# Kernel tuning notes

Measured on AMD Instinct MI355X. Metric: run time of the kernel, lower is better.

Reference implementation:

```python
import jax, jax.numpy as jnp
import numpy as np

N, E, D = 50000, 400000, 64
L, NA, NS = 5, 4, 3            # layers, num aggregators, num scalers
ATOM_C, ATOM_V = 9, 64         # OGB-style atom feature columns / vocab
BOND_C, BOND_V = 3, 8
EPS = 1e-5
AVG_LOG = float(np.log(9.0))   # avg_d['log'] = ln(avg_degree + 1), avg_degree = 8


def setup_inputs() -> dict:
    key = jax.random.key(0)
    ks = jax.random.split(key, 8)
    x = jax.random.randint(ks[0], (N, ATOM_C), 0, ATOM_V)
    edge_index = jax.random.randint(ks[1], (2, E), 0, N)
    edge_attr = jax.random.randint(ks[2], (E, BOND_C), 0, BOND_V)
    init = lambda k, shape, fan: (jax.random.normal(k, shape, jnp.float32) / np.sqrt(fan))
    atom_emb = init(ks[3], (ATOM_C, ATOM_V, D), D)
    bond_emb = init(ks[4], (BOND_C, BOND_V, D), D)
    pre_W = init(ks[5], (L, 3 * D, D), 3 * D)                 # pretrans: Linear(3D -> D)
    pre_b = jnp.zeros((L, D), jnp.float32)
    post_W = init(ks[6], (L, (NA * NS + 1) * D, D), (NA * NS + 1) * D)  # posttrans: Linear(13D -> D)
    post_b = jnp.zeros((L, D), jnp.float32)
    return dict(x=x, edge_index=edge_index, edge_attr=edge_attr,
                atom_emb=atom_emb, bond_emb=bond_emb,
                pre_W=pre_W, pre_b=pre_b, post_W=post_W, post_b=post_b)


def reference(x, edge_index, edge_attr, atom_emb, bond_emb, pre_W, pre_b, post_W, post_b):
    src, dst = edge_index[0], edge_index[1]  # PyG: x_j = x[edge_index[0]], x_i = x[edge_index[1]]
    # Encoders: sum of per-column categorical embeddings (OGB Atom/BondEncoder)
    h0 = atom_emb[jnp.arange(ATOM_C)[None, :], x].sum(axis=1)        # [N, D]
    e = bond_emb[jnp.arange(BOND_C)[None, :], edge_attr].sum(axis=1)  # [E, D]
    # message input cat([x_i, x_j, edge_attr]) -- identical for every layer since
    # PNAGNN.forward never feeds layer output back in as x (faithful to source)
    z2 = jnp.concatenate([h0[dst], h0[src], e], axis=-1)              # [E, 3D]
    deg = jax.ops.segment_sum(jnp.ones((E,), jnp.float32), dst, num_segments=N)
    degc = jnp.maximum(deg, 1.0)[:, None]
    log_deg = jnp.log(jnp.maximum(deg, 1.0) + 1.0)[:, None]           # guard deg=0 for attenuation
    amp = log_deg / AVG_LOG
    att = AVG_LOG / log_deg
    has = (deg > 0)[:, None]
    h_in = h0
    for l in range(L):
        m = z2 @ pre_W[l] + pre_b[l]                                  # pretrans (1 layer, no act)
        s_sum = jax.ops.segment_sum(m, dst, num_segments=N)
        mean = s_sum / degc
        mx = jnp.where(has, jax.ops.segment_max(m, dst, num_segments=N), 0.0)
        mn = jnp.where(has, jax.ops.segment_min(m, dst, num_segments=N), 0.0)
        mean_sq = jax.ops.segment_sum(m * m, dst, num_segments=N) / degc
        var = jax.nn.relu(mean_sq - mean * mean)
        std = jnp.sqrt(var + EPS)
        agg = jnp.concatenate([mean, mx, mn, std], axis=-1)           # [N, 4D]
        scaled = jnp.concatenate([agg, agg * amp, agg * att], axis=-1)  # [N, 12D]
        hcat = jnp.concatenate([scaled, h0], axis=-1)                 # [N, 13D]
        out = hcat @ post_W[l] + post_b[l]                            # posttrans (1 layer, no act)
        h = out + h_in                                                # PNAGNN residual
        h_in = h
    return h
```

## Files before the change

### kernel.cpp

```cpp
#include <hip/hip_runtime.h>
#include <hip/hip_bf16.h>

#define NN 50000
#define NE 400000
#define AVG_LOG_F 2.1972245773362196f
#define EPSV 1e-5f

typedef __hip_bfloat16 bf16;
typedef __attribute__((ext_vector_type(8))) short short8v;
typedef __attribute__((ext_vector_type(4))) float f32x4;
typedef __attribute__((ext_vector_type(2))) _Float16 h2v;

__device__ __forceinline__ float b2f(bf16 v){ return __bfloat162float(v); }
__device__ __forceinline__ bf16  f2b(float v){ return __float2bfloat16(v); }
__device__ __forceinline__ short f2s(float v){
  bf16 b = __float2bfloat16(v);
  short s; __builtin_memcpy(&s, &b, 2); return s;
}
__device__ __forceinline__ short f2h(float v){
  _Float16 h = (_Float16)v;
  short s; __builtin_memcpy(&s, &h, 2); return s;
}

__global__ void k_h0(const int* __restrict__ x, const float* __restrict__ aemb,
                     bf16* __restrict__ h0b){
  int idx = blockIdx.x * 256 + threadIdx.x;
  if (idx >= NN * 64) return;
  int n = idx >> 6, d = idx & 63;
  float acc = 0.f;
  #pragma unroll
  for (int c = 0; c < 9; ++c){
    int a = x[n * 9 + c];
    acc += aemb[(c * 64 + a) * 64 + d];
  }
  h0b[idx] = f2b(acc);
}

__global__ void k_deg_code(const int* __restrict__ ei, const int* __restrict__ ea,
                           int* __restrict__ deg, int* __restrict__ code){
  int e = blockIdx.x * 256 + threadIdx.x;
  if (e >= NE) return;
  int dst = ei[NE + e];
  atomicAdd(&deg[dst], 1);
  code[e] = ea[e * 3] + 8 * ea[e * 3 + 1] + 64 * ea[e * 3 + 2];
}

__global__ void k_scan1(const int* __restrict__ deg, int* __restrict__ rowptr,
                        int* __restrict__ part){
  __shared__ int s[256];
  int t = threadIdx.x, i = blockIdx.x * 256 + t;
  int v = (i < NN) ? deg[i] : 0;
  s[t] = v; __syncthreads();
  for (int off = 1; off < 256; off <<= 1){
    int xv = (t >= off) ? s[t - off] : 0;
    __syncthreads();
    s[t] += xv;
    __syncthreads();
  }
  if (i < NN) rowptr[i] = s[t] - v;
  if (t == 255) part[blockIdx.x] = s[255];
}

__global__ void k_scan2(int* __restrict__ part, int nblk){
  __shared__ int s[256];
  int t = threadIdx.x;
  int v = (t < nblk) ? part[t] : 0;
  s[t] = v; __syncthreads();
  for (int off = 1; off < 256; off <<= 1){
    int xv = (t >= off) ? s[t - off] : 0;
    __syncthreads();
    s[t] += xv;
    __syncthreads();
  }
  if (t < nblk) part[t] = s[t] - v;
}

__global__ void k_scan3(int* __restrict__ rowptr, const int* __restrict__ part,
                        const int* __restrict__ deg, float* __restrict__ amp,
                        float* __restrict__ att){
  int i = blockIdx.x * 256 + threadIdx.x;
  if (i < NN){
    rowptr[i] += part[blockIdx.x];
    int d = deg[i];
    float ld = logf((float)max(d, 1) + 1.0f);
    amp[i] = ld / AVG_LOG_F;
    att[i] = AVG_LOG_F / ld;
  }
  if (i == 0) rowptr[NN] = NE;
}

__global__ void k_scatter(const int* __restrict__ ei, const int* __restrict__ code,
                          const int* __restrict__ rowptr, int* __restrict__ cursor,
                          int2* __restrict__ sedge){
  int e = blockIdx.x * 256 + threadIdx.x;
  if (e >= NE) return;
  int dst = ei[NE + e];
  int pos = rowptr[dst] + atomicAdd(&cursor[dst], 1);
  int2 v; v.x = ei[e] * 1280; v.y = code[e] * 640;
  sedge[pos] = v;
}

__global__ void k_ctab(const float* __restrict__ bemb, const float* __restrict__ preW,
                       _Float16* __restrict__ CTp){
  __shared__ float et[64];
  int cb = blockIdx.x, l = blockIdx.y, t = threadIdx.x;
  int a0 = cb & 7, a1 = (cb >> 3) & 7, a2 = (cb >> 6) & 7;
  et[t] = bemb[(0 * 8 + a0) * 64 + t] + bemb[(1 * 8 + a1) * 64 + t] + bemb[(2 * 8 + a2) * 64 + t];
  __syncthreads();
  float acc = 0.f;
  const float* W = preW + (l * 192 + 128) * 64;
  for (int k = 0; k < 64; ++k) acc += et[k] * W[k * 64 + t];
  char* base = (char*)CTp + (size_t)cb * 640;
  if (l < 4) *(short*)(base + t * 8 + l * 2) = f2h(acc);
  else       *(short*)(base + 512 + t * 2)   = f2h(acc);
}

__global__ void k_wtk(const float* __restrict__ postW, bf16* __restrict__ WtKf){
  int idx = blockIdx.x * 256 + threadIdx.x;
  if (idx >= 40 * 12 * 64 * 8) return;
  int s   = idx / 6144;
  int rem = idx % 6144;
  int gw  = rem / 512;
  int lane = (rem % 512) / 8;
  int j   = idx & 7;
  int g = gw >> 2, w4 = gw & 3;
  int kp = s * 32 + (lane >> 4) * 8 + j;
  int l = kp >> 8, kl = kp & 255;
  int c = w4 * 16 + (lane & 15);
  WtKf[idx] = f2b(postW[((size_t)l * 832 + g * 256 + kl) * 64 + c]);
}

__global__ void k_wtpre896(const float* __restrict__ preW, const float* __restrict__ preb,
                           const float* __restrict__ postW, const float* __restrict__ postb,
                           bf16* __restrict__ Wtp, float* __restrict__ bias896){
  int idx = blockIdx.x * 256 + threadIdx.x;
  if (idx < 896 * 64){
    int gc = idx >> 6, k = idx & 63;
    float v;
    if (gc < 320){
      int l = gc >> 6, c = gc & 63;
      v = preW[(size_t)(l * 192 + k) * 64 + c];
    } else if (gc < 832){
      int q = gc - 320, d = q >> 3, l = q & 7;
      v = (l < 5) ? preW[(size_t)(l * 192 + 64 + k) * 64 + d] : 0.f;
    } else {
      int c = gc - 832;
      float a = 0.f;
      #pragma unroll
      for (int l = 0; l < 5; ++l) a += postW[(size_t)(l * 832 + 768 + k) * 64 + c];
      v = a + ((k == c) ? 1.f : 0.f);
    }
    Wtp[idx] = f2b(v);
  }
  if (idx < 896){
    float b;
    if (idx < 320)      b = preb[(idx >> 6) * 64 + (idx & 63)];
    else if (idx < 832) b = 0.f;
    else {
      float a = 0.f;
      #pragma unroll
      for (int l = 0; l < 5; ++l) a += postb[l * 64 + (idx - 832)];
      b = a;
    }
    bias896[idx] = b;
  }
}

__global__ __launch_bounds__(256) void k_ab_mfma(const bf16* __restrict__ h0b,
                                                 const bf16* __restrict__ Wtp,
                                                 const float* __restrict__ bias896,
                                                 char* __restrict__ ABU,
                                                 float* __restrict__ out){
  __shared__ bf16 As[128][72];
  __shared__ bf16 Bs[128][72];
  const int t = threadIdx.x;
  const int n0 = blockIdx.x * 128;
  const int gc0 = blockIdx.y * 128;
  const int lane = t & 63, wid = t >> 6;
  const int rw = wid * 32;
  const short* H  = (const short*)h0b;
  const short* Wp = (const short*)Wtp;

  #pragma unroll
  for (int i = 0; i < 4; ++i){
    int idx = t + i * 256;
    int r = idx >> 3, ko = (idx & 7) * 8;
    int n = n0 + r;
    short8v v = short8v{0,0,0,0,0,0,0,0};
    if (n < NN) v = *(const short8v*)(H + (size_t)n * 64 + ko);
    *(short8v*)&As[r][ko] = v;
  }
  #pragma unroll
  for (int i = 0; i < 4; ++i){
    int idx = t + i * 256;
    int cc = idx >> 3, ko = (idx & 7) * 8;
    *(short8v*)&Bs[cc][ko] = *(const short8v*)(Wp + (size_t)(gc0 + cc) * 64 + ko);
  }
  __syncthreads();

  f32x4 acc[2][8] = {};
  #pragma unroll
  for (int kk = 0; kk < 2; ++kk){
    short8v af0 = *(const short8v*)&As[rw + (lane & 15)][kk * 32 + (lane >> 4) * 8];
    short8v af1 = *(const short8v*)&As[rw + 16 + (lane & 15)][kk * 32 + (lane >> 4) * 8];
    #pragma unroll
    for (int j = 0; j < 8; ++j){
      short8v bfj = *(const short8v*)&Bs[j * 16 + (lane & 15)][kk * 32 + (lane >> 4) * 8];
      acc[0][j] = __builtin_amdgcn_mfma_f32_16x16x32_bf16(af0, bfj, acc[0][j], 0, 0, 0);
      acc[1][j] = __builtin_amdgcn_mfma_f32_16x16x32_bf16(af1, bfj, acc[1][j], 0, 0, 0);
    }
  }

  #pragma unroll
  for (int i = 0; i < 2; ++i){
    #pragma unroll
    for (int r = 0; r < 4; ++r){
      int n = n0 + rw + i * 16 + (lane >> 4) * 4 + r;
      if (n >= NN) continue;
      char* nb = ABU + (size_t)n * 1280;
      #pragma unroll
      for (int j = 0; j < 8; ++j){
        int gc = gc0 + j * 16 + (lane & 15);
        float v = acc[i][j][r] + bias896[gc];
        if (gc < 320){
          *(short*)(nb + gc * 2) = f2h(v);
        } else if (gc < 832){
          int q = gc - 320, dd = q >> 3, l = q & 7;
          if (l < 4)       *(short*)(nb + 640 + dd * 8 + l * 2) = f2h(v);
          else if (l == 4) *(short*)(nb + 1152 + dd * 2)        = f2h(v);
        } else {
          out[(size_t)n * 64 + (gc - 832)] = v;
        }
      }
    }
  }
}

__global__ __launch_bounds__(1024, 2) void k_gather(const char* __restrict__ ABU,
                                                    const char* __restrict__ CTp,
                                                    const int* __restrict__ rowptr,
                                                    const int2* __restrict__ sedge,
                                                    const bf16* __restrict__ WtKf,
                                                    const float* __restrict__ amp,
                                                    const float* __restrict__ att,
                                                    float* __restrict__ out){
  __shared__ __align__(16) short ag[16][1288];
  const int t = threadIdx.x, lane = t & 63, wid = t >> 6;
  const int n = blockIdx.x * 16 + wid;
  const char* AB8 = ABU + 640;
  const char* AB2 = ABU + 1152;
  const char* CT8 = CTp;
  const char* CT2 = CTp + 512;

  int r0 = rowptr[n], r1 = rowptr[n + 1];
  float s[5]  = {0.f, 0.f, 0.f, 0.f, 0.f};
  float sq[5] = {0.f, 0.f, 0.f, 0.f, 0.f};
  const _Float16 FLO = (_Float16)(-65504.f);
  const _Float16 FHI = (_Float16)( 65504.f);
  h2v mx01 = h2v{FLO, FLO}, mx23 = h2v{FLO, FLO};
  h2v mn01 = h2v{FHI, FHI}, mn23 = h2v{FHI, FHI};
  float mx4 = -65504.f, mn4 = 65504.f;

  union U8 { uint2 u; h2v h[2]; };
  const int l8 = lane * 8, l2 = lane * 2;

  for (int j = r0; j < r1; j += 4){
    int rem = r1 - j;
    int2 e0 = sedge[j];
    int2 e1 = (rem > 1) ? sedge[j + 1] : e0;
    int2 e2 = (rem > 2) ? sedge[j + 2] : e0;
    int2 e3 = (rem > 3) ? sedge[j + 3] : e0;
    U8 a0, a1, a2, a3, c0, c1, c2, c3;
    unsigned short b0, b1, b2, b3, d0, d1, d2, d3;
    a0.u = *(const uint2*)(AB8 + e0.x + l8);  b0 = *(const unsigned short*)(AB2 + e0.x + l2);
    c0.u = *(const uint2*)(CT8 + e0.y + l8);  d0 = *(const unsigned short*)(CT2 + e0.y + l2);
    a1.u = *(const uint2*)(AB8 + e1.x + l8);  b1 = *(const unsigned short*)(AB2 + e1.x + l2);
    c1.u = *(const uint2*)(CT8 + e1.y + l8);  d1 = *(const unsigned short*)(CT2 + e1.y + l2);
    a2.u = *(const uint2*)(AB8 + e2.x + l8);  b2 = *(const unsigned short*)(AB2 + e2.x + l2);
    c2.u = *(const uint2*)(CT8 + e2.y + l8);  d2 = *(const unsigned short*)(CT2 + e2.y + l2);
    a3.u = *(const uint2*)(AB8 + e3.x + l8);  b3 = *(const unsigned short*)(AB2 + e3.x + l2);
    c3.u = *(const uint2*)(CT8 + e3.y + l8);  d3 = *(const unsigned short*)(CT2 + e3.y + l2);

    #define EDGE_ACC(A, C, BL, DL) {                                \
      h2v t01 = A.h[0] + C.h[0];                                    \
      h2v t23 = A.h[1] + C.h[1];                                    \
      _Float16 hb, hd;                                              \
      __builtin_memcpy(&hb, &BL, 2);                                \
      __builtin_memcpy(&hd, &DL, 2);                                \
      float f4 = (float)(hb + hd);                                  \
      mx01 = __builtin_elementwise_max(mx01, t01);                  \
      mx23 = __builtin_elementwise_max(mx23, t23);                  \
      mn01 = __builtin_elementwise_min(mn01, t01);                  \
      mn23 = __builtin_elementwise_min(mn23, t23);                  \
      mx4 = fmaxf(mx4, f4); mn4 = fminf(mn4, f4);                   \
      float f0 = (float)t01[0], f1 = (float)t01[1];                 \
      float f2 = (float)t23[0], f3 = (float)t23[1];                 \
      s[0] += f0; sq[0] = fmaf(f0, f0, sq[0]);                      \
      s[1] += f1; sq[1] = fmaf(f1, f1, sq[1]);                      \
      s[2] += f2; sq[2] = fmaf(f2, f2, sq[2]);                      \
      s[3] += f3; sq[3] = fmaf(f3, f3, sq[3]);                      \
      s[4] += f4; sq[4] = fmaf(f4, f4, sq[4]);                      \
    }
    EDGE_ACC(a0, c0, b0, d0);
    if (rem > 1) EDGE_ACC(a1, c1, b1, d1);
    if (rem > 2) EDGE_ACC(a2, c2, b2, d2);
    if (rem > 3) EDGE_ACC(a3, c3, b3, d3);
    #undef EDGE_ACC
  }

  float mx[5] = {(float)mx01[0], (float)mx01[1], (float)mx23[0], (float)mx23[1], mx4};
  float mn[5] = {(float)mn01[0], (float)mn01[1], (float)mn23[0], (float)mn23[1], mn4};

  int d = r1 - r0;
  float degc = (float)((d > 0) ? d : 1);
  const char* nb = ABU + (size_t)n * 1280;
  #pragma unroll
  for (int l = 0; l < 5; ++l){
    _Float16 Kh; __builtin_memcpy(&Kh, nb + l * 128 + lane * 2, 2);
    float K = (float)Kh;
    float mean = ((float)d * K + s[l]) / degc;
    float MX = (d > 0) ? (K + mx[l]) : 0.f;
    float MN = (d > 0) ? (K + mn[l]) : 0.f;
    float mu = s[l] / degc;
    float var = fmaxf(sq[l] / degc - mu * mu, 0.f);
    float sd = sqrtf(var + EPSV);
    ag[wid][l * 256 + lane]       = f2s(mean);
    ag[wid][l * 256 + 64 + lane]  = f2s(MX);
    ag[wid][l * 256 + 128 + lane] = f2s(MN);
    ag[wid][l * 256 + 192 + lane] = f2s(sd);
  }
  __syncthreads();

  if (wid >= 4) return;

  const char* pb = (const char*)WtKf + wid * 1024 + lane * 16;
  const short* agrow = &ag[lane & 15][(lane >> 4) * 8];
  f32x4 acc[3] = {};
  short8v Bx[3], By[3];

  #define LOADB(dst, sidx) { \
    _Pragma("unroll") for (int g = 0; g < 3; ++g) \
      dst[g] = *(const short8v*)(pb + (size_t)(sidx) * 12288 + g * 4096); }
  #define MFMA3(af, B) { \
    _Pragma("unroll") for (int g = 0; g < 3; ++g) \
      acc[g] = __builtin_amdgcn_mfma_f32_16x16x32_bf16(af, B[g], acc[g], 0, 0, 0); }

  LOADB(Bx, 0);
  for (int k = 0; k < 19; ++k){
    LOADB(By, 2 * k + 1);
    short8v af0 = *(const short8v*)(agrow + (2 * k) * 32);
    MFMA3(af0, Bx);
    LOADB(Bx, 2 * k + 2);
    short8v af1 = *(const short8v*)(agrow + (2 * k + 1) * 32);
    MFMA3(af1, By);
  }
  LOADB(By, 39);
  {
    short8v af0 = *(const short8v*)(agrow + 38 * 32);
    MFMA3(af0, Bx);
    short8v af1 = *(const short8v*)(agrow + 39 * 32);
    MFMA3(af1, By);
  }
  #undef LOADB
  #undef MFMA3

  #pragma unroll
  for (int r = 0; r < 4; ++r){
    int row = (lane >> 4) * 4 + r;
    int nn = blockIdx.x * 16 + row;
    float am = amp[nn], at = att[nn];
    int c = wid * 16 + (lane & 15);
    out[(size_t)nn * 64 + c] += acc[0][r] + am * acc[1][r] + at * acc[2][r];
  }
}

extern "C" void kernel_launch(void* const* d_in, const int* in_sizes, int n_in,
                              void* d_out, int out_size, void* d_ws, size_t ws_size,
                              hipStream_t stream){
  const int*   x     = (const int*)d_in[0];
  const int*   ei    = (const int*)d_in[1];
  const int*   ea    = (const int*)d_in[2];
  const float* aemb  = (const float*)d_in[3];
  const float* bemb  = (const float*)d_in[4];
  const float* preW  = (const float*)d_in[5];
  const float* preb  = (const float*)d_in[6];
  const float* postW = (const float*)d_in[7];
  const float* postb = (const float*)d_in[8];
  float* out = (float*)d_out;

  char* p = (char*)d_ws;
  auto alloc = [&](size_t bytes) -> char* {
    char* r = p;
    p += (bytes + 255) & ~(size_t)255;
    return r;
  };
  bf16*      h0b     = (bf16*)     alloc((size_t)NN * 64 * 2);
  char*      ABU     = (char*)     alloc((size_t)NN * 1280);
  int*       deg     = (int*)      alloc((size_t)NN * 4);
  int*       rowptr  = (int*)      alloc((size_t)(NN + 1) * 4);
  int*       cursor  = (int*)      alloc((size_t)NN * 4);
  float*     amp     = (float*)    alloc((size_t)NN * 4);
  float*     att     = (float*)    alloc((size_t)NN * 4);
  int*       code    = (int*)      alloc((size_t)NE * 4);
  int2*      sedge   = (int2*)     alloc((size_t)NE * 8);
  _Float16*  CTp     = (_Float16*) alloc((size_t)512 * 640);
  int*       part    = (int*)      alloc((size_t)256 * 4);
  bf16*      WtKf    = (bf16*)     alloc((size_t)40 * 12 * 64 * 8 * 2);
  bf16*      Wtp     = (bf16*)     alloc((size_t)896 * 64 * 2);
  float*     bias896 = (float*)    alloc((size_t)896 * 4);
  if ((size_t)(p - (char*)d_ws) > ws_size) return;

  hipMemsetAsync(deg, 0, (size_t)NN * 4, stream);
  hipMemsetAsync(cursor, 0, (size_t)NN * 4, stream);

  k_h0<<<dim3((NN * 64 + 255) / 256), 256, 0, stream>>>(x, aemb, h0b);
  k_deg_code<<<dim3((NE + 255) / 256), 256, 0, stream>>>(ei, ea, deg, code);
  int nblk = (NN + 255) / 256;
  k_scan1<<<dim3(nblk), 256, 0, stream>>>(deg, rowptr, part);
  k_scan2<<<dim3(1), 256, 0, stream>>>(part, nblk);
  k_scan3<<<dim3(nblk), 256, 0, stream>>>(rowptr, part, deg, amp, att);
  k_scatter<<<dim3((NE + 255) / 256), 256, 0, stream>>>(ei, code, rowptr, cursor, sedge);
  k_ctab<<<dim3(512, 5), 64, 0, stream>>>(bemb, preW, CTp);
  k_wtk<<<dim3((40 * 12 * 64 * 8 + 255) / 256), 256, 0, stream>>>(postW, WtKf);
  k_wtpre896<<<dim3((896 * 64 + 255) / 256), 256, 0, stream>>>(preW, preb, postW, postb,
                                                               Wtp, bias896);
  k_ab_mfma<<<dim3((NN + 127) / 128, 7), 256, 0, stream>>>(h0b, Wtp, bias896, ABU, out);
  k_gather<<<dim3(NN / 16), 1024, 0, stream>>>(ABU, (const char*)CTp, rowptr, sedge,
                                               WtKf, amp, att, out);
}
```

Baseline: 267.6 us.

## Split posttrans K-loop across all waves with LDS reduction

New measurement: 270.3 us. No clear change (+1.0%).

```diff
diff --git a/kernel.cpp b/kernel.cpp
--- a/kernel.cpp
+++ b/kernel.cpp
@@ -331,10 +331,9 @@
   }
   __syncthreads();
 
-  if (wid >= 4) return;
-
-  const char* pb = (const char*)WtKf + wid * 1024 + lane * 16;
-  const short* agrow = &ag[lane & 15][(lane >> 4) * 8];
+  const int cs = wid & 3, kq = wid >> 2;
+  const char* pb = (const char*)WtKf + cs * 1024 + (size_t)kq * 10 * 12288 + lane * 16;
+  const short* agq = &ag[lane & 15][(lane >> 4) * 8] + kq * 10 * 32;
   f32x4 acc[3] = {};
   short8v Bx[3], By[3];
 
@@ -346,23 +345,36 @@
       acc[g] = __builtin_amdgcn_mfma_f32_16x16x32_bf16(af, B[g], acc[g], 0, 0, 0); }
 
   LOADB(Bx, 0);
-  for (int k = 0; k < 19; ++k){
+  #pragma unroll
+  for (int k = 0; k < 5; ++k){
     LOADB(By, 2 * k + 1);
-    short8v af0 = *(const short8v*)(agrow + (2 * k) * 32);
+    short8v af0 = *(const short8v*)(agq + (2 * k) * 32);
     MFMA3(af0, Bx);
-    LOADB(Bx, 2 * k + 2);
-    short8v af1 = *(const short8v*)(agrow + (2 * k + 1) * 32);
-    MFMA3(af1, By);
-  }
-  LOADB(By, 39);
-  {
-    short8v af0 = *(const short8v*)(agrow + 38 * 32);
-    MFMA3(af0, Bx);
-    short8v af1 = *(const short8v*)(agrow + 39 * 32);
+    if (k < 4) LOADB(Bx, 2 * k + 2);
+    short8v af1 = *(const short8v*)(agq + (2 * k + 1) * 32);
     MFMA3(af1, By);
   }
   #undef LOADB
   #undef MFMA3
+
+  __syncthreads();
+  f32x4* red = (f32x4*)&ag[0][0];
+  if (wid >= 4){
+    #pragma unroll
+    for (int g = 0; g < 3; ++g)
+      red[((wid - 4) * 3 + g) * 64 + lane] = acc[g];
+    __syncthreads();
+    return;
+  }
+  __syncthreads();
+  #pragma unroll
+  for (int q = 0; q < 3; ++q){
+    #pragma unroll
+    for (int g = 0; g < 3; ++g){
+      f32x4 o = red[((q * 4 + wid) * 3 + g) * 64 + lane];
+      acc[g][0] += o[0]; acc[g][1] += o[1]; acc[g][2] += o[2]; acc[g][3] += o[3];
+    }
+  }
 
   #pragma unroll
   for (int r = 0; r < 4; ++r){
```

## Merge setup kernels and interleave five per-layer gather values into 12-byte records

Applied to the files above, without the earlier changes.

New measurement: 285.7 us. 6.8% more time.

```diff
diff --git a/kernel.cpp b/kernel.cpp
--- a/kernel.cpp
+++ b/kernel.cpp
@@ -11,7 +11,9 @@
 typedef __attribute__((ext_vector_type(4))) float f32x4;
 typedef __attribute__((ext_vector_type(2))) _Float16 h2v;
 
-__device__ __forceinline__ float b2f(bf16 v){ return __bfloat162float(v); }
+struct __attribute__((aligned(4))) u12 { unsigned x, y, z; };
+union P12 { u12 u; h2v h[3]; };
+
 __device__ __forceinline__ bf16  f2b(float v){ return __float2bfloat16(v); }
 __device__ __forceinline__ short f2s(float v){
   bf16 b = __float2bfloat16(v);
@@ -22,18 +24,102 @@
   short s; __builtin_memcpy(&s, &h, 2); return s;
 }
 
-__global__ void k_h0(const int* __restrict__ x, const float* __restrict__ aemb,
-                     bf16* __restrict__ h0b){
-  int idx = blockIdx.x * 256 + threadIdx.x;
-  if (idx >= NN * 64) return;
-  int n = idx >> 6, d = idx & 63;
-  float acc = 0.f;
-  #pragma unroll
-  for (int c = 0; c < 9; ++c){
-    int a = x[n * 9 + c];
-    acc += aemb[(c * 64 + a) * 64 + d];
-  }
-  h0b[idx] = f2b(acc);
+#define PB_H0  12500
+#define PB_Z   12891
+#define PB_CT  13403
+#define PB_WK  14363
+#define PB_END 14587
+
+__global__ __launch_bounds__(256) void k_pre(const int* __restrict__ x,
+                                             const float* __restrict__ aemb,
+                                             const float* __restrict__ bemb,
+                                             const float* __restrict__ preW,
+                                             const float* __restrict__ preb,
+                                             const float* __restrict__ postW,
+                                             const float* __restrict__ postb,
+                                             bf16* __restrict__ h0b,
+                                             int* __restrict__ deg, int* __restrict__ cursor,
+                                             char* __restrict__ CTp,
+                                             bf16* __restrict__ WtKf,
+                                             bf16* __restrict__ Wtp,
+                                             float* __restrict__ bias896){
+  __shared__ float et[64];
+  const int b = blockIdx.x, t = threadIdx.x;
+  if (b < PB_H0){
+    int idx = b * 256 + t;
+    int n = idx >> 6, d = idx & 63;
+    float acc = 0.f;
+    #pragma unroll
+    for (int c = 0; c < 9; ++c){
+      int a = x[n * 9 + c];
+      acc += aemb[(c * 64 + a) * 64 + d];
+    }
+    h0b[idx] = f2b(acc);
+  } else if (b < PB_Z){
+    int idx = (b - PB_H0) * 256 + t;
+    if (idx < NN) deg[idx] = 0;
+    else if (idx < 2 * NN) cursor[idx - NN] = 0;
+  } else if (b < PB_CT){
+    int cb = b - PB_Z;
+    if (t < 64){
+      int a0 = cb & 7, a1 = (cb >> 3) & 7, a2 = (cb >> 6) & 7;
+      et[t] = bemb[a0 * 64 + t] + bemb[(8 + a1) * 64 + t] + bemb[(16 + a2) * 64 + t];
+    }
+    __syncthreads();
+    char* base = CTp + (size_t)cb * 1024;
+    for (int w = t; w < 320; w += 256){
+      int l = w >> 6, dd = w & 63;
+      float acc = 0.f;
+      const float* W = preW + (l * 192 + 128) * 64;
+      for (int k = 0; k < 64; ++k) acc += et[k] * W[k * 64 + dd];
+      *(short*)(base + dd * 12 + l * 2) = f2h(acc);
+    }
+    if (t < 64) *(short*)(base + t * 12 + 10) = 0;
+  } else if (b < PB_WK){
+    int idx = (b - PB_CT) * 256 + t;
+    int s   = idx / 6144;
+    int rem = idx % 6144;
+    int gw  = rem / 512;
+    int lane = (rem % 512) / 8;
+    int j   = idx & 7;
+    int g = gw >> 2, w4 = gw & 3;
+    int kp = s * 32 + (lane >> 4) * 8 + j;
+    int l = kp >> 8, kl = kp & 255;
+    int c = w4 * 16 + (lane & 15);
+    WtKf[idx] = f2b(postW[((size_t)l * 832 + g * 256 + kl) * 64 + c]);
+  } else {
+    int idx = (b - PB_WK) * 256 + t;
+    {
+      int gc = idx >> 6, k = idx & 63;
+      float v;
+      if (gc < 320){
+        int l = gc >> 6, c = gc & 63;
+        v = preW[(size_t)(l * 192 + k) * 64 + c];
+      } else if (gc < 832){
+        int q = gc - 320, d = q >> 3, l = q & 7;
+        v = (l < 5) ? preW[(size_t)(l * 192 + 64 + k) * 64 + d] : 0.f;
+      } else {
+        int c = gc - 832;
+        float a = 0.f;
+        #pragma unroll
+        for (int l = 0; l < 5; ++l) a += postW[(size_t)(l * 832 + 768 + k) * 64 + c];
+        v = a + ((k == c) ? 1.f : 0.f);
+      }
+      Wtp[idx] = f2b(v);
+    }
+    if (idx < 896){
+      float bb;
+      if (idx < 320)      bb = preb[(idx >> 6) * 64 + (idx & 63)];
+      else if (idx < 832) bb = 0.f;
+      else {
+        float a = 0.f;
+        #pragma unroll
+        for (int l = 0; l < 5; ++l) a += postb[l * 64 + (idx - 832)];
+        bb = a;
+      }
+      bias896[idx] = bb;
+    }
+  }
 }
 
 __global__ void k_deg_code(const int* __restrict__ ei, const int* __restrict__ ea,
@@ -96,74 +182,8 @@
   if (e >= NE) return;
   int dst = ei[NE + e];
   int pos = rowptr[dst] + atomicAdd(&cursor[dst], 1);
-  int2 v; v.x = ei[e] * 1280; v.y = code[e] * 640;
+  int2 v; v.x = ei[e] * 2048 + 1024; v.y = code[e] * 1024;
   sedge[pos] = v;
-}
-
-__global__ void k_ctab(const float* __restrict__ bemb, const float* __restrict__ preW,
-                       _Float16* __restrict__ CTp){
-  __shared__ float et[64];
-  int cb = blockIdx.x, l = blockIdx.y, t = threadIdx.x;
-  int a0 = cb & 7, a1 = (cb >> 3) & 7, a2 = (cb >> 6) & 7;
-  et[t] = bemb[(0 * 8 + a0) * 64 + t] + bemb[(1 * 8 + a1) * 64 + t] + bemb[(2 * 8 + a2) * 64 + t];
-  __syncthreads();
-  float acc = 0.f;
-  const float* W = preW + (l * 192 + 128) * 64;
-  for (int k = 0; k < 64; ++k) acc += et[k] * W[k * 64 + t];
-  char* base = (char*)CTp + (size_t)cb * 640;
-  if (l < 4) *(short*)(base + t * 8 + l * 2) = f2h(acc);
-  else       *(short*)(base + 512 + t * 2)   = f2h(acc);
-}
-
-__global__ void k_wtk(const float* __restrict__ postW, bf16* __restrict__ WtKf){
-  int idx = blockIdx.x * 256 + threadIdx.x;
-  if (idx >= 40 * 12 * 64 * 8) return;
-  int s   = idx / 6144;
-  int rem = idx % 6144;
-  int gw  = rem / 512;
-  int lane = (rem % 512) / 8;
-  int j   = idx & 7;
-  int g = gw >> 2, w4 = gw & 3;
-  int kp = s * 32 + (lane >> 4) * 8 + j;
-  int l = kp >> 8, kl = kp & 255;
-  int c = w4 * 16 + (lane & 15);
-  WtKf[idx] = f2b(postW[((size_t)l * 832 + g * 256 + kl) * 64 + c]);
-}
-
-__global__ void k_wtpre896(const float* __restrict__ preW, const float* __restrict__ preb,
-                           const float* __restrict__ postW, const float* __restrict__ postb,
-                           bf16* __restrict__ Wtp, float* __restrict__ bias896){
-  int idx = blockIdx.x * 256 + threadIdx.x;
-  if (idx < 896 * 64){
-    int gc = idx >> 6, k = idx & 63;
-    float v;
-    if (gc < 320){
-      int l = gc >> 6, c = gc & 63;
-      v = preW[(size_t)(l * 192 + k) * 64 + c];
-    } else if (gc < 832){
-      int q = gc - 320, d = q >> 3, l = q & 7;
-      v = (l < 5) ? preW[(size_t)(l * 192 + 64 + k) * 64 + d] : 0.f;
-    } else {
-      int c = gc - 832;
-      float a = 0.f;
-      #pragma unroll
-      for (int l = 0; l < 5; ++l) a += postW[(size_t)(l * 832 + 768 + k) * 64 + c];
-      v = a + ((k == c) ? 1.f : 0.f);
-    }
-    Wtp[idx] = f2b(v);
-  }
-  if (idx < 896){
-    float b;
-    if (idx < 320)      b = preb[(idx >> 6) * 64 + (idx & 63)];
-    else if (idx < 832) b = 0.f;
-    else {
-      float a = 0.f;
-      #pragma unroll
-      for (int l = 0; l < 5; ++l) a += postb[l * 64 + (idx - 832)];
-      b = a;
-    }
-    bias896[idx] = b;
-  }
 }
 
 __global__ __launch_bounds__(256) void k_ab_mfma(const bf16* __restrict__ h0b,
@@ -217,7 +237,7 @@
     for (int r = 0; r < 4; ++r){
       int n = n0 + rw + i * 16 + (lane >> 4) * 4 + r;
       if (n >= NN) continue;
-      char* nb = ABU + (size_t)n * 1280;
+      char* nb = ABU + (size_t)n * 2048;
       #pragma unroll
       for (int j = 0; j < 8; ++j){
         int gc = gc0 + j * 16 + (lane & 15);
@@ -226,8 +246,7 @@
           *(short*)(nb + gc * 2) = f2h(v);
         } else if (gc < 832){
           int q = gc - 320, dd = q >> 3, l = q & 7;
-          if (l < 4)       *(short*)(nb + 640 + dd * 8 + l * 2) = f2h(v);
-          else if (l == 4) *(short*)(nb + 1152 + dd * 2)        = f2h(v);
+          if (l < 6) *(short*)(nb + 1024 + dd * 12 + l * 2) = f2h(v);
         } else {
           out[(size_t)n * 64 + (gc - 832)] = v;
         }
@@ -247,22 +266,16 @@
   __shared__ __align__(16) short ag[16][1288];
   const int t = threadIdx.x, lane = t & 63, wid = t >> 6;
   const int n = blockIdx.x * 16 + wid;
-  const char* AB8 = ABU + 640;
-  const char* AB2 = ABU + 1152;
-  const char* CT8 = CTp;
-  const char* CT2 = CTp + 512;
 
   int r0 = rowptr[n], r1 = rowptr[n + 1];
   float s[5]  = {0.f, 0.f, 0.f, 0.f, 0.f};
   float sq[5] = {0.f, 0.f, 0.f, 0.f, 0.f};
   const _Float16 FLO = (_Float16)(-65504.f);
   const _Float16 FHI = (_Float16)( 65504.f);
-  h2v mx01 = h2v{FLO, FLO}, mx23 = h2v{FLO, FLO};
-  h2v mn01 = h2v{FHI, FHI}, mn23 = h2v{FHI, FHI};
-  float mx4 = -65504.f, mn4 = 65504.f;
-
-  union U8 { uint2 u; h2v h[2]; };
-  const int l8 = lane * 8, l2 = lane * 2;
+  h2v mx01 = h2v{FLO, FLO}, mx23 = h2v{FLO, FLO}, mx45 = h2v{FLO, FLO};
+  h2v mn01 = h2v{FHI, FHI}, mn23 = h2v{FHI, FHI}, mn45 = h2v{FHI, FHI};
+
+  const int l12 = lane * 12;
 
   for (int j = r0; j < r1; j += 4){
     int rem = r1 - j;
@@ -270,50 +283,48 @@
     int2 e1 = (rem > 1) ? sedge[j + 1] : e0;
     int2 e2 = (rem > 2) ? sedge[j + 2] : e0;
     int2 e3 = (rem > 3) ? sedge[j + 3] : e0;
-    U8 a0, a1, a2, a3, c0, c1, c2, c3;
-    unsigned short b0, b1, b2, b3, d0, d1, d2, d3;
-    a0.u = *(const uint2*)(AB8 + e0.x + l8);  b0 = *(const unsigned short*)(AB2 + e0.x + l2);
-    c0.u = *(const uint2*)(CT8 + e0.y + l8);  d0 = *(const unsigned short*)(CT2 + e0.y + l2);
-    a1.u = *(const uint2*)(AB8 + e1.x + l8);  b1 = *(const unsigned short*)(AB2 + e1.x + l2);
-    c1.u = *(const uint2*)(CT8 + e1.y + l8);  d1 = *(const unsigned short*)(CT2 + e1.y + l2);
-    a2.u = *(const uint2*)(AB8 + e2.x + l8);  b2 = *(const unsigned short*)(AB2 + e2.x + l2);
-    c2.u = *(const uint2*)(CT8 + e2.y + l8);  d2 = *(const unsigned short*)(CT2 + e2.y + l2);
-    a3.u = *(const uint2*)(AB8 + e3.x + l8);  b3 = *(const unsigned short*)(AB2 + e3.x + l2);
-    c3.u = *(const uint2*)(CT8 + e3.y + l8);  d3 = *(const unsigned short*)(CT2 + e3.y + l2);
-
-    #define EDGE_ACC(A, C, BL, DL) {                                \
+    P12 a0, a1, a2, a3, c0, c1, c2, c3;
+    a0.u = *(const u12*)(ABU + e0.x + l12);
+    c0.u = *(const u12*)(CTp + e0.y + l12);
+    a1.u = *(const u12*)(ABU + e1.x + l12);
+    c1.u = *(const u12*)(CTp + e1.y + l12);
+    a2.u = *(const u12*)(ABU + e2.x + l12);
+    c2.u = *(const u12*)(CTp + e2.y + l12);
+    a3.u = *(const u12*)(ABU + e3.x + l12);
+    c3.u = *(const u12*)(CTp + e3.y + l12);
+
+    #define EDGE_ACC(A, C) {                                        \
       h2v t01 = A.h[0] + C.h[0];                                    \
       h2v t23 = A.h[1] + C.h[1];                                    \
-      _Float16 hb, hd;                                              \
-      __builtin_memcpy(&hb, &BL, 2);                                \
-      __builtin_memcpy(&hd, &DL, 2);                                \
-      float f4 = (float)(hb + hd);                                  \
+      h2v t45 = A.h[2] + C.h[2];                                    \
       mx01 = __builtin_elementwise_max(mx01, t01);                  \
       mx23 = __builtin_elementwise_max(mx23, t23);                  \
+      mx45 = __builtin_elementwise_max(mx45, t45);                  \
       mn01 = __builtin_elementwise_min(mn01, t01);                  \
       mn23 = __builtin_elementwise_min(mn23, t23);                  \
-      mx4 = fmaxf(mx4, f4); mn4 = fminf(mn4, f4);                   \
+      mn45 = __builtin_elementwise_min(mn45, t45);                  \
       float f0 = (float)t01[0], f1 = (float)t01[1];                 \
       float f2 = (float)t23[0], f3 = (float)t23[1];                 \
+      float f4 = (float)t45[0];                                     \
       s[0] += f0; sq[0] = fmaf(f0, f0, sq[0]);                      \
       s[1] += f1; sq[1] = fmaf(f1, f1, sq[1]);                      \
       s[2] += f2; sq[2] = fmaf(f2, f2, sq[2]);                      \
       s[3] += f3; sq[3] = fmaf(f3, f3, sq[3]);                      \
       s[4] += f4; sq[4] = fmaf(f4, f4, sq[4]);                      \
     }
-    EDGE_ACC(a0, c0, b0, d0);
-    if (rem > 1) EDGE_ACC(a1, c1, b1, d1);
-    if (rem > 2) EDGE_ACC(a2, c2, b2, d2);
-    if (rem > 3) EDGE_ACC(a3, c3, b3, d3);
+    EDGE_ACC(a0, c0);
+    if (rem > 1) EDGE_ACC(a1, c1);
+    if (rem > 2) EDGE_ACC(a2, c2);
+    if (rem > 3) EDGE_ACC(a3, c3);
     #undef EDGE_ACC
   }
 
-  float mx[5] = {(float)mx01[0], (float)mx01[1], (float)mx23[0], (float)mx23[1], mx4};
-  float mn[5] = {(float)mn01[0], (float)mn01[1], (float)mn23[0], (float)mn23[1], mn4};
+  float mx[5] = {(float)mx01[0], (float)mx01[1], (float)mx23[0], (float)mx23[1], (float)mx45[0]};
+  float mn[5] = {(float)mn01[0], (float)mn01[1], (float)mn23[0], (float)mn23[1], (float)mn45[0]};
 
   int d = r1 - r0;
   float degc = (float)((d > 0) ? d : 1);
-  const char* nb = ABU + (size_t)n * 1280;
+  const char* nb = ABU + (size_t)n * 2048;
   #pragma unroll
   for (int l = 0; l < 5; ++l){
     _Float16 Kh; __builtin_memcpy(&Kh, nb + l * 128 + lane * 2, 2);
@@ -395,7 +406,7 @@
     return r;
   };
   bf16*      h0b     = (bf16*)     alloc((size_t)NN * 64 * 2);
-  char*      ABU     = (char*)     alloc((size_t)NN * 1280);
+  char*      ABU     = (char*)     alloc((size_t)NN * 2048);
   int*       deg     = (int*)      alloc((size_t)NN * 4);
   int*       rowptr  = (int*)      alloc((size_t)(NN + 1) * 4);
   int*       cursor  = (int*)      alloc((size_t)NN * 4);
@@ -403,27 +414,21 @@
   float*     att     = (float*)    alloc((size_t)NN * 4);
   int*       code    = (int*)      alloc((size_t)NE * 4);
   int2*      sedge   = (int2*)     alloc((size_t)NE * 8);
-  _Float16*  CTp     = (_Float16*) alloc((size_t)512 * 640);
+  char*      CTp     = (char*)     alloc((size_t)512 * 1024);
   int*       part    = (int*)      alloc((size_t)256 * 4);
   bf16*      WtKf    = (bf16*)     alloc((size_t)40 * 12 * 64 * 8 * 2);
   bf16*      Wtp     = (bf16*)     alloc((size_t)896 * 64 * 2);
   float*     bias896 = (float*)    alloc((size_t)896 * 4);
   if ((size_t)(p - (char*)d_ws) > ws_size) return;
 
-  hipMemsetAsync(deg, 0, (size_t)NN * 4, stream);
-  hipMemsetAsync(cursor, 0, (size_t)NN * 4, stream);
-
-  k_h0<<<dim3((NN * 64 + 255) / 256), 256, 0, stream>>>(x, aemb, h0b);
+  k_pre<<<dim3(PB_END), 256, 0, stream>>>(x, aemb, bemb, preW, preb, postW, postb,
+                                          h0b, deg, cursor, CTp, WtKf, Wtp, bias896);
   k_deg_code<<<dim3((NE + 255) / 256), 256, 0, stream>>>(ei, ea, deg, code);
   int nblk = (NN + 255) / 256;
   k_scan1<<<dim3(nblk), 256, 0, stream>>>(deg, rowptr, part);
   k_scan2<<<dim3(1), 256, 0, stream>>>(part, nblk);
   k_scan3<<<dim3(nblk), 256, 0, stream>>>(rowptr, part, deg, amp, att);
   k_scatter<<<dim3((NE + 255) / 256), 256, 0, stream>>>(ei, code, rowptr, cursor, sedge);
-  k_ctab<<<dim3(512, 5), 64, 0, stream>>>(bemb, preW, CTp);
-  k_wtk<<<dim3((40 * 12 * 64 * 8 + 255) / 256), 256, 0, stream>>>(postW, WtKf);
-  k_wtpre896<<<dim3((896 * 64 + 255) / 256), 256, 0, stream>>>(preW, preb, postW, postb,
-                                                               Wtp, bias896);
   k_ab_mfma<<<dim3((NN + 127) / 128, 7), 256, 0, stream>>>(h0b, Wtp, bias896, ABU, out);
   k_gather<<<dim3(NN / 16), 1024, 0, stream>>>(ABU, (const char*)CTp, rowptr, sedge,
                                                WtKf, amp, att, out);
```
